# Performance work log

Hardware: AMD Instinct MI355X
Metric: run time of the kernel (lower is better)

Reference implementation:

```python
import jax, jax.numpy as jnp
import numpy as np

NEG_INF = -1e30  # safe -inf surrogate to avoid nan in logsumexp


def _ctc_loss_sum(log_probs, labels, input_lengths, label_lengths):
    # log_probs: (T, N, C) already log-softmaxed; blank = 0
    T, N, C = log_probs.shape
    S = labels.shape[1]
    L = 2 * S + 1  # extended label sequence: blank-interleaved

    # extended labels: [blank, y1, blank, y2, ..., blank]
    ext = jnp.zeros((N, L), dtype=jnp.int32).at[:, 1::2].set(labels.astype(jnp.int32))
    # gather emission log-probs for extended labels: (T, N, L)
    lp_ext = jnp.take_along_axis(log_probs, jnp.broadcast_to(ext[None], (T, N, L)), axis=2)

    # transition from l-2 allowed only for non-blank labels differing from ext[l-2]
    ext_m2 = jnp.pad(ext, ((0, 0), (2, 0)), constant_values=-1)[:, :L]
    allow_skip = (ext != 0) & (ext != ext_m2)  # (N, L)

    # alpha at t=0
    alpha0 = jnp.full((N, L), NEG_INF, dtype=log_probs.dtype)
    alpha0 = alpha0.at[:, 0].set(lp_ext[0, :, 0])
    alpha0 = alpha0.at[:, 1].set(jnp.where(label_lengths > 0, lp_ext[0, :, 1], NEG_INF))

    def step(alpha, t_and_lp):
        t, lp_t = t_and_lp  # lp_t: (N, L)
        a1 = jnp.pad(alpha, ((0, 0), (1, 0)), constant_values=NEG_INF)[:, :L]
        a2 = jnp.pad(alpha, ((0, 0), (2, 0)), constant_values=NEG_INF)[:, :L]
        a2 = jnp.where(allow_skip, a2, NEG_INF)
        m = jnp.maximum(jnp.maximum(alpha, a1), a2)
        lse = m + jnp.log(jnp.exp(alpha - m) + jnp.exp(a1 - m) + jnp.exp(a2 - m))
        new = jnp.where(m > NEG_INF / 2, lse + lp_t, NEG_INF)
        # freeze alpha past each sequence's input length
        alpha = jnp.where((t < input_lengths)[:, None], new, alpha)
        return alpha, None

    alpha, _ = jax.lax.scan(step, alpha0, (jnp.arange(1, T), lp_ext[1:]))

    # log-likelihood = logsumexp(alpha[2*Sl], alpha[2*Sl - 1])
    idx = (2 * label_lengths).astype(jnp.int32)
    a_last = jnp.take_along_axis(alpha, idx[:, None], axis=1)[:, 0]
    a_prev = jnp.take_along_axis(alpha, jnp.maximum(idx - 1, 0)[:, None], axis=1)[:, 0]
    a_prev = jnp.where(label_lengths > 0, a_prev, NEG_INF)
    m = jnp.maximum(a_last, a_prev)
    ll = m + jnp.log(jnp.exp(a_last - m) + jnp.exp(a_prev - m))
    loss = -ll
    # zero_infinity=True: replace infinite losses with 0
    loss = jnp.where(loss < -NEG_INF / 2, loss, 0.0)
    return jnp.sum(loss)


def setup_inputs() -> dict:
    T, N, C, S = 512, 32, 4000, 64
    key = jax.random.key(0)
    k1, k2 = jax.random.split(key)
    inputs = jax.random.normal(k1, (T, N, C), dtype=jnp.float32)
    labels = jax.random.randint(k2, (N, S), 1, C, dtype=jnp.int32)  # exclude blank=0
    input_lengths = jnp.full((N,), T, dtype=jnp.int32)
    label_lengths = jnp.full((N,), S, dtype=jnp.int32)
    return {"inputs": inputs, "labels": labels,
            "input_lengths": input_lengths, "label_lengths": label_lengths}


def reference(inputs, labels, input_lengths, label_lengths):
    log_probs = jax.nn.log_softmax(inputs, axis=2)
    return _ctc_loss_sum(log_probs, labels, input_lengths, label_lengths)
```

## Files before the change

### kernel.cpp

```cpp
#include <hip/hip_runtime.h>

#define LN2 0.6931471805599453f

constexpr int T = 512, N = 32, C = 4000, S = 64;
constexpr int TN   = T * N;
constexpr int ROWF = 68;
constexpr int CT   = 16;
constexpr int NCF  = 16;
constexpr int NCB  = 16;
constexpr int NCG  = 32;

__global__ __launch_bounds__(256) void k_softmax_probs(
    const float* __restrict__ x, const int* __restrict__ labels,
    float* __restrict__ pp, float* __restrict__ ee)
{
    int row  = blockIdx.x * 4 + (threadIdx.x >> 6);
    int lane = threadIdx.x & 63;
    const float*  rp  = x + (size_t)row * C;
    const float4* rp4 = reinterpret_cast<const float4*>(rp);

    float m = -INFINITY, s = 0.f;
    #pragma unroll
    for (int k = 0; k < 15; ++k) {
        float4 v = rp4[lane + 64 * k];
        float mv = fmaxf(fmaxf(v.x, v.y), fmaxf(v.z, v.w));
        float s4 = __expf(v.x - mv) + __expf(v.y - mv) +
                   __expf(v.z - mv) + __expf(v.w - mv);
        float nm = fmaxf(m, mv);
        s = s * __expf(m - nm) + s4 * __expf(mv - nm);
        m = nm;
    }
    if (lane < 40) {
        float4 v = rp4[960 + lane];
        float mv = fmaxf(fmaxf(v.x, v.y), fmaxf(v.z, v.w));
        float s4 = __expf(v.x - mv) + __expf(v.y - mv) +
                   __expf(v.z - mv) + __expf(v.w - mv);
        float nm = fmaxf(m, mv);
        s = s * __expf(m - nm) + s4 * __expf(mv - nm);
        m = nm;
    }
    for (int off = 32; off; off >>= 1) {
        float om = __shfl_xor(m, off), os = __shfl_xor(s, off);
        float nm = fmaxf(m, om);
        s = s * __expf(m - nm) + os * __expf(om - nm);
        m = nm;
    }
    float logZ = m + __logf(s);

    int t = row >> 5, n = row & 31;
    int c  = labels[n * S + lane];
    float zb = rp[0];
    float zl = rp[c];

    float wm = zl;
    for (int off = 32; off; off >>= 1) wm = fmaxf(wm, __shfl_xor(wm, off));
    wm = fmaxf(wm, zb);
    float pm = __expf(wm - logZ);
    int e = (int)(__float_as_uint(pm) >> 23) - 127;

    float* outp = pp + ((size_t)n * T + t) * ROWF;
    outp[1 + lane] = ldexpf(__expf(zl - logZ), -e);
    if (lane == 0) {
        outp[0] = ldexpf(__expf(zb - logZ), -e);
        ee[n * T + t] = (float)e;
    }
}

__device__ __forceinline__ float dpp_shr1_zero(float x) {
    int r = __builtin_amdgcn_update_dpp(0, __float_as_int(x),
                                        0x138 , 0xf, 0xf, false);
    return __int_as_float(r);
}
__device__ __forceinline__ float dpp_shl1_zero(float x) {
    int r = __builtin_amdgcn_update_dpp(0, __float_as_int(x),
                                        0x130 , 0xf, 0xf, false);
    return __int_as_float(r);
}
template <int CTRL>
__device__ __forceinline__ float dpp_max_step(float x) {
    int t = __builtin_amdgcn_update_dpp(__float_as_int(x), __float_as_int(x),
                                        CTRL, 0xf, 0xf, false);
    return fmaxf(x, __int_as_float(t));
}
__device__ __forceinline__ float wave_max_bcast(float x) {
    x = dpp_max_step<0xB1>(x);  x = dpp_max_step<0x4E>(x);
    x = dpp_max_step<0x141>(x); x = dpp_max_step<0x140>(x);
    x = dpp_max_step<0x142>(x); x = dpp_max_step<0x143>(x);
    return __int_as_float(__builtin_amdgcn_readlane(__float_as_int(x), 63));
}

__global__ __launch_bounds__(128) void k_ctc_alpha(
    const float* __restrict__ pp, const float* __restrict__ ee,
    const int* __restrict__ labels,
    const int* __restrict__ input_len, const int* __restrict__ label_len,
    float* __restrict__ loss_out)
{
    __shared__ __align__(16) float ldsF[2][CT][ROWF];
    __shared__ __align__(16) float ldsB[2][CT][ROWF];
    __shared__ float gj[132];
    const int n = blockIdx.x;
    const int wid = threadIdx.x >> 6, lane = threadIdx.x & 63;
    const int Tin = input_len[n], Sl = label_len[n];
    const float* bp = pp + (size_t)n * T * ROWF;
    const bool hot = (Tin == T);

    const int li   = labels[n * S + lane];
    const int lim1 = lane ? labels[n * S + lane - 1] : -1;
    const float skf  = (lane > 0 && li != 0 && li != lim1) ? 1.f : 0.f;
    const float skUf = dpp_shr1_zero(skf);
    const float skk  = skf * skUf;
    const float skD  = dpp_shl1_zero(skf);

    asm volatile("s_waitcnt vmcnt(0)" ::: "memory");
    __builtin_amdgcn_sched_barrier(0);

    float a0 = 0.f, a1 = 0.f, aX = 0.f;
    int SH = 0;

#define ISSUE_F(cc) do {                                                      \
    const float* cp_ = bp + (size_t)(cc) * CT * ROWF;                         \
    if (lane < 17) {                                                          \
        _Pragma("unroll")                                                     \
        for (int d_ = 0; d_ < CT; ++d_)                                       \
            __builtin_amdgcn_global_load_lds(cp_ + (size_t)d_ * ROWF + lane * 4, \
                                             &ldsF[(cc) & 1][d_][0], 16, 0, 0);\
    } } while (0)
#define ISSUE_B(cc) do {                                                      \
    const float* cp_ = bp + (size_t)(496 - 16 * (cc)) * ROWF;                 \
    if (lane < 17) {                                                          \
        _Pragma("unroll")                                                     \
        for (int d_ = 0; d_ < CT; ++d_)                                       \
            __builtin_amdgcn_global_load_lds(cp_ + (size_t)d_ * ROWF + lane * 4, \
                                             &ldsB[(cc) & 1][d_][0], 16, 0, 0);\
    } } while (0)

#define PAIRS(B, D) do {                                                      \
    const float* R0_ = &ldsF[B][D][0];                                        \
    const float* R1_ = &ldsF[B][(D) + 1][0];                                  \
    float cb1 = R0_[0], cl1 = R0_[1 + lane];                                  \
    float cb2 = R1_[0], cl2 = R1_[1 + lane];                                  \
    float clU = dpp_shr1_zero(cl1);                                           \
    float W   = clU * cl2;                                                    \
    float A   = cb1 * cb2;                                                    \
    float B_  = clU * cb2;                                                    \
    float Cc  = A + B_;                                                       \
    float D_  = skUf * B_;                                                    \
    float s1  = cb1 + cl1;                                                    \
    float E   = s1 * cl2;                                                     \
    float F   = cl1 * cl2;                                                    \
    float G   = skf * W;                                                      \
    float H   = fmaf(skf, F + W, cb1 * cl2);                                  \
    float I   = skk * W;                                                      \
    float Y0  = cl1 * cb2;                                                    \
    float Y1  = s1 * cb2;                                                     \
    float Y2  = skf * Y0;                                                     \
    float p1  = dpp_shr1_zero(a1);                                            \
    float p0  = dpp_shr1_zero(a0);                                            \
    float p2  = dpp_shr1_zero(p1);                                            \
    float n0  = fmaf(p0, B_, a0 * A) + fmaf(p2, D_, p1 * Cc);                 \
    float n1  = fmaf(a1, F, a0 * E) + fmaf(p2, I, fmaf(p1, H, p0 * G));       \
    float nX  = fmaf(a1, Y1, aX * A) + fmaf(p1, Y2, a0 * Y0);                 \
    a0 = n0; a1 = n1; aX = nX;                                                \
} while (0)

#define WINDOW4(B, D0) do {                                                   \
    a0 = ldexpf(a0, kA); a1 = ldexpf(a1, kA); aX = ldexpf(aX, kA);            \
    SH += kA;                                                                 \
    float gnow_ = fmaxf(fmaxf(a0, a1), aX);                                   \
    PAIRS(B, D0);                                                             \
    gs = dpp_max_step<0xB1>(gs);  gs = dpp_max_step<0x4E>(gs);                \
    PAIRS(B, (D0) + 2);                                                       \
    gs = dpp_max_step<0x141>(gs); gs = dpp_max_step<0x140>(gs);               \
    PAIRS(B, (D0) + 4);                                                       \
    gs = dpp_max_step<0x142>(gs); gs = dpp_max_step<0x143>(gs);               \
    PAIRS(B, (D0) + 6);                                                       \
    {   unsigned b_ = (unsigned)__builtin_amdgcn_readlane(__float_as_int(gs), 63); \
        int e_ = (int)(b_ >> 23) - 127;                                       \
        kA = (b_ == 0u) ? 0 : (105 - e_ - kA);                                \
    }                                                                         \
    gs = gnow_;                                                               \
} while (0)

#define BSTEP(B, D) do {                                                      \
    const float* R_ = &ldsB[B][D][0];                                         \
    float cb_ = R_[0], cl_ = R_[1 + lane];                                    \
    float cD_ = dpp_shl1_zero(cl_);                         \
    float d1_ = dpp_shl1_zero(g1);                           \
    float d0s_ = dpp_shl1_zero(g0);                          \
    float d0_ = (lane == 63) ? gX : d0s_;             \
    float t1_ = skD * cD_;                                                    \
    float cg_ = cl_ * g1;                                                     \
    float ng0 = fmaf(cb_, g0, cg_);                                           \
    float ng1 = fmaf(t1_, d1_, fmaf(cb_, d0_, cg_));                          \
    float ngX = cb_ * gX;                                                     \
    g0 = ng0; g1 = ng1; gX = ngX;                                             \
} while (0)

#define BWIN(B, D0) do {                                                      \
    g0 = ldexpf(g0, kB); g1 = ldexpf(g1, kB); gX = ldexpf(gX, kB);            \
    SHb += kB;                                                                \
    float gnow_ = fmaxf(fmaxf(g0, g1), gX);                                   \
    BSTEP(B, (D0) + 7); BSTEP(B, (D0) + 6);                                   \
    gsb = dpp_max_step<0xB1>(gsb);  gsb = dpp_max_step<0x4E>(gsb);            \
    BSTEP(B, (D0) + 5); BSTEP(B, (D0) + 4);                                   \
    gsb = dpp_max_step<0x141>(gsb); gsb = dpp_max_step<0x140>(gsb);           \
    BSTEP(B, (D0) + 3); BSTEP(B, (D0) + 2);                                   \
    gsb = dpp_max_step<0x142>(gsb); gsb = dpp_max_step<0x143>(gsb);           \
    BSTEP(B, (D0) + 1); BSTEP(B, (D0));                                       \
    {   unsigned b_ = (unsigned)__builtin_amdgcn_readlane(__float_as_int(gsb), 63); \
        int e_ = (int)(b_ >> 23) - 127;                                       \
        kB = (b_ == 0u) ? 0 : (100 - e_ - kB);                                \
    }                                                                         \
    gsb = gnow_;                                                              \
} while (0)

    if (wid == 0) {
        if (hot) {
            int kA = 0; float gs = 0.f;
            ISSUE_F(0); ISSUE_F(1);
            asm volatile("s_waitcnt vmcnt(16)" ::: "memory");
            __builtin_amdgcn_sched_barrier(0);
            a0 = (lane == 0) ? ldsF[0][0][0] : 0.f;
            a1 = (lane == 0 && Sl > 0) ? ldsF[0][0][1] : 0.f;
            {
                float cb = ldsF[0][1][0], cl = ldsF[0][1][1 + lane];
                float p1 = dpp_shr1_zero(a1);
                float n0 = (a0 + p1) * cb;
                float n1 = fmaf(skf, p1, a0 + a1) * cl;
                float nX = (aX + a1) * cb;
                a0 = n0; a1 = n1; aX = nX;
            }
            PAIRS(0, 2); PAIRS(0, 4); PAIRS(0, 6);
            {   float g = wave_max_bcast(fmaxf(fmaxf(a0, a1), aX));
                unsigned b = __float_as_uint(g);
                int k0 = (b == 0u) ? 0 : (105 - ((int)(b >> 23) - 127));
                a0 = ldexpf(a0, k0); a1 = ldexpf(a1, k0); aX = ldexpf(aX, k0);
                SH += k0; kA = 0;
                gs = fmaxf(fmaxf(a0, a1), aX);
            }
            WINDOW4(0, 8);
            __builtin_amdgcn_sched_barrier(0);
            ISSUE_F(2);
            for (int c = 1; c < NCF; ++c) {
                if (c < NCF - 1) { asm volatile("s_waitcnt vmcnt(16)" ::: "memory"); }
                else             { asm volatile("s_waitcnt vmcnt(0)"  ::: "memory"); }
                __builtin_amdgcn_sched_barrier(0);
                int buf = c & 1;
                WINDOW4(buf, 0);
                WINDOW4(buf, 8);
                if (c + 2 < NCF) {
                    __builtin_amdgcn_sched_barrier(0);
                    ISSUE_F(c + 2);
                }
            }
        } else {
#define GSTEP(cc, dd) do {                                                    \
    float cb_ = ldsF[(cc) & 1][dd][0];                                        \
    float cl_ = ldsF[(cc) & 1][dd][1 + lane];                                 \
    float p1_ = dpp_shr1_zero(a1);                                            \
    float na0_ = (a0 + p1_) * cb_;                                            \
    float na1_ = fmaf(skf, p1_, a0 + a1) * cl_;                               \
    float naX_ = (aX + a1) * cb_;                                             \
    int t_ = (cc) * CT + (dd);                                                \
    bool act_ = (unsigned)(t_ - 1) < (unsigned)(Tin - 1);                     \
    a0 = act_ ? na0_ : a0;                                                    \
    a1 = act_ ? na1_ : a1;                                                    \
    aX = act_ ? naX_ : aX;                                                    \
    if (((dd) & 3) == 3) {                                                    \
        float g_ = wave_max_bcast(fmaxf(a0, fmaxf(a1, aX)));                  \
        unsigned b_ = __float_as_uint(g_);                                    \
        int k_ = (b_ == 0u) ? 0 : (100 - ((int)(b_ >> 23) - 127));            \
        a0 = ldexpf(a0, k_); a1 = ldexpf(a1, k_); aX = ldexpf(aX, k_);        \
        SH += k_;                                                             \
    }                                                                         \
} while (0)
            ISSUE_F(0); ISSUE_F(1);
            asm volatile("s_waitcnt vmcnt(16)" ::: "memory");
            __builtin_amdgcn_sched_barrier(0);
            a0 = (lane == 0) ? ldsF[0][0][0] : 0.f;
            a1 = (lane == 0 && Sl > 0) ? ldsF[0][0][1] : 0.f;
            #pragma unroll
            for (int d = 1; d < CT; ++d) GSTEP(0, d);
            __builtin_amdgcn_sched_barrier(0);
            ISSUE_F(2);
            for (int c = 1; c < NCG; ++c) {
                if (c < NCG - 1) { asm volatile("s_waitcnt vmcnt(16)" ::: "memory"); }
                else             { asm volatile("s_waitcnt vmcnt(0)"  ::: "memory"); }
                __builtin_amdgcn_sched_barrier(0);
                #pragma unroll
                for (int d = 0; d < CT; ++d) GSTEP(c, d);
                if (c + 2 < NCG) {
                    __builtin_amdgcn_sched_barrier(0);
                    ISSUE_F(c + 2);
                }
            }
#undef GSTEP
        }
    } else if (hot) {
        float g0 = (lane == Sl) ? 1.f : 0.f;
        float g1 = (Sl > 0 && lane == Sl - 1) ? 1.f : 0.f;
        float gX = (Sl >= S && lane == 63) ? 1.f : 0.f;
        int SHb = 0, kB = 0;
        float gsb = fmaxf(fmaxf(g0, g1), gX);

        ISSUE_B(0); ISSUE_B(1);
        for (int c = 0; c < NCB; ++c) {
            if (c < NCB - 1) { asm volatile("s_waitcnt vmcnt(16)" ::: "memory"); }
            else             { asm volatile("s_waitcnt vmcnt(0)"  ::: "memory"); }
            __builtin_amdgcn_sched_barrier(0);
            int buf = c & 1;
            BWIN(buf, 8);
            BWIN(buf, 0);
            if (c + 2 < NCB) {
                __builtin_amdgcn_sched_barrier(0);
                ISSUE_B(c + 2);
            }
        }
        gj[2 * lane]     = ldexpf(g0, -120);
        gj[2 * lane + 1] = ldexpf(g1, -120);
        if (lane == 63) {
            gj[128] = ldexpf(gX, -120);
            gj[130] = (float)SHb;
        }
    }

    __syncthreads();
    if (wid != 0) return;

    float se = 0.f;
    #pragma unroll
    for (int j = 0; j < 8; ++j) {
        int idx = lane + 64 * j;
        float ev = ee[n * T + idx];
        se += (idx < Tin) ? ev : 0.f;
    }
    for (int off = 32; off; off >>= 1) se += __shfl_xor(se, off);

    if (hot) {
        float term = a0 * gj[2 * lane] + a1 * gj[2 * lane + 1];
        if (lane == 63) term = fmaf(aX, gj[128], term);
        for (int off = 32; off; off >>= 1) term += __shfl_xor(term, off);
        if (lane == 0) {
            float SHb = gj[130];
            float ll2  = log2f(term) - (float)SH - SHb + 120.f + se;
            float loss = -ll2 * LN2;
            if (!(loss < 5e29f)) loss = 0.f;
            loss_out[n] = loss;
        }
    } else {
        float a_last = (Sl >= S) ? __shfl(aX, 63) : __shfl(a0, Sl);
        float a_prev_raw = __shfl(a1, (Sl > 0) ? (Sl - 1) : 0);
        float a_prev = (Sl > 0) ? a_prev_raw : 0.f;
        if (lane == 0) {
            float sum  = a_last + a_prev;
            float ll2  = log2f(sum) - (float)SH + se;
            float loss = -ll2 * LN2;
            if (!(loss < 5e29f)) loss = 0.f;
            loss_out[n] = loss;
        }
    }
#undef BWIN
#undef BSTEP
#undef WINDOW4
#undef PAIRS
#undef ISSUE_F
#undef ISSUE_B
}

__global__ __launch_bounds__(64) void k_reduce(
    const float* __restrict__ loss, float* __restrict__ out)
{
    int lane = threadIdx.x;
    float v = (lane < N) ? loss[lane] : 0.f;
    for (int off = 32; off; off >>= 1) v += __shfl_xor(v, off);
    if (lane == 0) out[0] = v;
}

extern "C" void kernel_launch(void* const* d_in, const int* in_sizes, int n_in,
                              void* d_out, int out_size, void* d_ws, size_t ws_size,
                              hipStream_t stream) {
    const float* x       = (const float*)d_in[0];
    const int*   labels  = (const int*)d_in[1];
    const int*   in_len  = (const int*)d_in[2];
    const int*   lab_len = (const int*)d_in[3];
    float* out  = (float*)d_out;
    float* pp   = (float*)d_ws;
    float* ee   = pp + (size_t)TN * ROWF + 256;
    float* loss = ee + TN;

    k_softmax_probs<<<TN / 4, 256, 0, stream>>>(x, labels, pp, ee);
    k_ctc_alpha<<<N, 128, 0, stream>>>(pp, ee, labels, in_len, lab_len, loss);
    k_reduce<<<1, 64, 0, stream>>>(loss, out);
}
```

Measured before the change: 77.57 us.

## Overlap backward CTC recursion with softmax via phased kernels

```diff
diff --git a/kernel.cpp b/kernel.cpp
--- a/kernel.cpp
+++ b/kernel.cpp
@@ -6,16 +6,36 @@
 constexpr int TN   = T * N;
 constexpr int ROWF = 68;
 constexpr int CT   = 16;
-constexpr int NCF  = 16;
-constexpr int NCB  = 16;
-constexpr int NCG  = 32;
-
-__global__ __launch_bounds__(256) void k_softmax_probs(
+constexpr int CTB  = 8;
+constexpr int QROWS = 4096;
+
+__device__ __forceinline__ float dpp_shr1_zero(float x) {
+    int r = __builtin_amdgcn_update_dpp(0, __float_as_int(x),
+                                        0x138 , 0xf, 0xf, false);
+    return __int_as_float(r);
+}
+__device__ __forceinline__ float dpp_shl1_zero(float x) {
+    int r = __builtin_amdgcn_update_dpp(0, __float_as_int(x),
+                                        0x130 , 0xf, 0xf, false);
+    return __int_as_float(r);
+}
+template <int CTRL>
+__device__ __forceinline__ float dpp_max_step(float x) {
+    int t = __builtin_amdgcn_update_dpp(__float_as_int(x), __float_as_int(x),
+                                        CTRL, 0xf, 0xf, false);
+    return fmaxf(x, __int_as_float(t));
+}
+__device__ __forceinline__ float wave_max_bcast(float x) {
+    x = dpp_max_step<0xB1>(x);  x = dpp_max_step<0x4E>(x);
+    x = dpp_max_step<0x141>(x); x = dpp_max_step<0x140>(x);
+    x = dpp_max_step<0x142>(x); x = dpp_max_step<0x143>(x);
+    return __int_as_float(__builtin_amdgcn_readlane(__float_as_int(x), 63));
+}
+
+__device__ __forceinline__ void softmax_row(
     const float* __restrict__ x, const int* __restrict__ labels,
-    float* __restrict__ pp, float* __restrict__ ee)
+    float* __restrict__ pp, float* __restrict__ ee, int row, int lane)
 {
-    int row  = blockIdx.x * 4 + (threadIdx.x >> 6);
-    int lane = threadIdx.x & 63;
     const float*  rp  = x + (size_t)row * C;
     const float4* rp4 = reinterpret_cast<const float4*>(rp);
 
@@ -66,41 +86,115 @@
     }
 }
 
-__device__ __forceinline__ float dpp_shr1_zero(float x) {
-    int r = __builtin_amdgcn_update_dpp(0, __float_as_int(x),
-                                        0x138 , 0xf, 0xf, false);
-    return __int_as_float(r);
-}
-__device__ __forceinline__ float dpp_shl1_zero(float x) {
-    int r = __builtin_amdgcn_update_dpp(0, __float_as_int(x),
-                                        0x130 , 0xf, 0xf, false);
-    return __int_as_float(r);
-}
-template <int CTRL>
-__device__ __forceinline__ float dpp_max_step(float x) {
-    int t = __builtin_amdgcn_update_dpp(__float_as_int(x), __float_as_int(x),
-                                        CTRL, 0xf, 0xf, false);
-    return fmaxf(x, __int_as_float(t));
-}
-__device__ __forceinline__ float wave_max_bcast(float x) {
-    x = dpp_max_step<0xB1>(x);  x = dpp_max_step<0x4E>(x);
-    x = dpp_max_step<0x141>(x); x = dpp_max_step<0x140>(x);
-    x = dpp_max_step<0x142>(x); x = dpp_max_step<0x143>(x);
-    return __int_as_float(__builtin_amdgcn_readlane(__float_as_int(x), 63));
-}
-
-__global__ __launch_bounds__(128) void k_ctc_alpha(
+__global__ __launch_bounds__(256) void k_phase(
+    const float* __restrict__ x, const int* __restrict__ labels,
+    float* __restrict__ pp, float* __restrict__ ee, float* __restrict__ gst,
+    const int* __restrict__ in_len, const int* __restrict__ lab_len,
+    int qrow0, int ttop, int first)
+{
+    __shared__ __align__(16) float ldsB[4][2][CTB][ROWF];
+    const int wid = threadIdx.x >> 6, lane = threadIdx.x & 63;
+
+    if (blockIdx.x >= 8) {
+        softmax_row(x, labels, pp, ee,
+                    qrow0 + ((int)blockIdx.x - 8) * 4 + wid, lane);
+        return;
+    }
+    if (ttop < 0) return;
+    const int n = blockIdx.x * 4 + wid;
+    const int Tin = in_len[n], Sl = lab_len[n];
+    if (Tin != T) return;
+    const float* bp = pp + (size_t)n * T * ROWF;
+
+    const int li = labels[n * S + lane];
+    const int lim1 = lane ? labels[n * S + lane - 1] : -1;
+    const float skf = (lane > 0 && li != 0 && li != lim1) ? 1.f : 0.f;
+    const float skD = dpp_shl1_zero(skf);
+
+    float* st = gst + n * 136;
+    float g0, g1, gX;
+    int SHb;
+    if (first) {
+        g0 = (lane == Sl) ? 1.f : 0.f;
+        g1 = (Sl > 0 && lane == Sl - 1) ? 1.f : 0.f;
+        gX = (Sl >= S && lane == 63) ? 1.f : 0.f;
+        SHb = 0;
+    } else {
+        float2 g = *reinterpret_cast<const float2*>(&st[2 * lane]);
+        g0 = g.x; g1 = g.y;
+        gX = (lane == 63) ? st[128] : 0.f;
+        SHb = (int)st[129];
+    }
+    asm volatile("s_waitcnt vmcnt(0)" ::: "memory");
+    __builtin_amdgcn_sched_barrier(0);
+
+#define ISSUEB(cc) do {                                                       \
+    const float* cp_ = bp + (size_t)(ttop - 7 - 8 * (cc)) * ROWF;             \
+    if (lane < 17) {                                                          \
+        _Pragma("unroll")                                                     \
+        for (int d_ = 0; d_ < CTB; ++d_)                                      \
+            __builtin_amdgcn_global_load_lds(cp_ + (size_t)d_ * ROWF + lane * 4, \
+                                             &ldsB[wid][(cc) & 1][d_][0], 16, 0, 0); \
+    } } while (0)
+
+#define BSTEPP(B, D) do {                                                     \
+    const float* R_ = &ldsB[wid][B][D][0];                                    \
+    float cb_ = R_[0], cl_ = R_[1 + lane];                                    \
+    float cD_ = dpp_shl1_zero(cl_);                         \
+    float d1_ = dpp_shl1_zero(g1);                           \
+    float d0s_ = dpp_shl1_zero(g0);                          \
+    float d0_ = (lane == 63) ? gX : d0s_;                                     \
+    float cg_ = cl_ * g1;                                                     \
+    float ng0 = fmaf(cb_, g0, cg_);                                           \
+    float ng1 = fmaf(skD * cD_, d1_, fmaf(cb_, d0_, cg_));                    \
+    float ngX = cb_ * gX;                                                     \
+    g0 = ng0; g1 = ng1; gX = ngX;                                             \
+} while (0)
+
+#define BRENORM do {                                                          \
+    float g_ = wave_max_bcast(fmaxf(g0, fmaxf(g1, gX)));                      \
+    unsigned b_ = __float_as_uint(g_);                                        \
+    int k_ = (b_ == 0u) ? 0 : (100 - ((int)(b_ >> 23) - 127));                \
+    g0 = ldexpf(g0, k_); g1 = ldexpf(g1, k_); gX = ldexpf(gX, k_);            \
+    SHb += k_;                                                                \
+} while (0)
+
+    ISSUEB(0); ISSUEB(1);
+    for (int c = 0; c < 16; ++c) {
+        if (c < 15) { asm volatile("s_waitcnt vmcnt(8)" ::: "memory"); }
+        else        { asm volatile("s_waitcnt vmcnt(0)" ::: "memory"); }
+        __builtin_amdgcn_sched_barrier(0);
+        int buf = c & 1;
+        BSTEPP(buf, 7); BSTEPP(buf, 6); BSTEPP(buf, 5); BSTEPP(buf, 4);
+        BRENORM;
+        BSTEPP(buf, 3); BSTEPP(buf, 2); BSTEPP(buf, 1); BSTEPP(buf, 0);
+        BRENORM;
+        if (c + 2 < 16) {
+            __builtin_amdgcn_sched_barrier(0);
+            ISSUEB(c + 2);
+        }
+    }
+
+    float2 gv; gv.x = g0; gv.y = g1;
+    *reinterpret_cast<float2*>(&st[2 * lane]) = gv;
+    if (lane == 63) { st[128] = gX; st[129] = (float)SHb; }
+#undef BRENORM
+#undef BSTEPP
+#undef ISSUEB
+}
+
+__global__ __launch_bounds__(128) void k_final(
     const float* __restrict__ pp, const float* __restrict__ ee,
-    const int* __restrict__ labels,
-    const int* __restrict__ input_len, const int* __restrict__ label_len,
+    float* __restrict__ gst, const int* __restrict__ labels,
+    const int* __restrict__ in_len, const int* __restrict__ lab_len,
     float* __restrict__ loss_out)
 {
     __shared__ __align__(16) float ldsF[2][CT][ROWF];
-    __shared__ __align__(16) float ldsB[2][CT][ROWF];
+    __shared__ __align__(16) float ldsT[2][CT][ROWF];
     __shared__ float gj[132];
     const int n = blockIdx.x;
     const int wid = threadIdx.x >> 6, lane = threadIdx.x & 63;
-    const int Tin = input_len[n], Sl = label_len[n];
+    const int Tin = in_len[n], Sl = lab_len[n];
     const float* bp = pp + (size_t)n * T * ROWF;
     const bool hot = (Tin == T);
 
@@ -111,9 +205,6 @@
     const float skk  = skf * skUf;
     const float skD  = dpp_shl1_zero(skf);
 
-    asm volatile("s_waitcnt vmcnt(0)" ::: "memory");
-    __builtin_amdgcn_sched_barrier(0);
-
     float a0 = 0.f, a1 = 0.f, aX = 0.f;
     int SH = 0;
 
@@ -123,15 +214,15 @@
         _Pragma("unroll")                                                     \
         for (int d_ = 0; d_ < CT; ++d_)                                       \
             __builtin_amdgcn_global_load_lds(cp_ + (size_t)d_ * ROWF + lane * 4, \
-                                             &ldsF[(cc) & 1][d_][0], 16, 0, 0);\
+                                             &ldsF[(cc) & 1][d_][0], 16, 0, 0); \
     } } while (0)
-#define ISSUE_B(cc) do {                                                      \
-    const float* cp_ = bp + (size_t)(496 - 16 * (cc)) * ROWF;                 \
+#define ISSUE_T(cc) do {                                                      \
+    const float* cp_ = bp + (size_t)(112 - 16 * (cc)) * ROWF;                 \
     if (lane < 17) {                                                          \
         _Pragma("unroll")                                                     \
         for (int d_ = 0; d_ < CT; ++d_)                                       \
             __builtin_amdgcn_global_load_lds(cp_ + (size_t)d_ * ROWF + lane * 4, \
-                                             &ldsB[(cc) & 1][d_][0], 16, 0, 0);\
+                                             &ldsT[(cc) & 1][d_][0], 16, 0, 0); \
     } } while (0)
 
 #define PAIRS(B, D) do {                                                      \
@@ -181,38 +272,29 @@
     gs = gnow_;                                                               \
 } while (0)
 
-#define BSTEP(B, D) do {                                                      \
-    const float* R_ = &ldsB[B][D][0];                                         \
+#define BSTEPT(B, D) do {                                                     \
+    const float* R_ = &ldsT[B][D][0];                                         \
     float cb_ = R_[0], cl_ = R_[1 + lane];                                    \
-    float cD_ = dpp_shl1_zero(cl_);                         \
-    float d1_ = dpp_shl1_zero(g1);                           \
-    float d0s_ = dpp_shl1_zero(g0);                          \
-    float d0_ = (lane == 63) ? gX : d0s_;             \
-    float t1_ = skD * cD_;                                                    \
+    float cD_ = dpp_shl1_zero(cl_);                                           \
+    float d1_ = dpp_shl1_zero(g1);                                            \
+    float d0s_ = dpp_shl1_zero(g0);                                           \
+    float d0_ = (lane == 63) ? gX : d0s_;                                     \
     float cg_ = cl_ * g1;                                                     \
     float ng0 = fmaf(cb_, g0, cg_);                                           \
-    float ng1 = fmaf(t1_, d1_, fmaf(cb_, d0_, cg_));                          \
+    float ng1 = fmaf(skD * cD_, d1_, fmaf(cb_, d0_, cg_));                    \
     float ngX = cb_ * gX;                                                     \
     g0 = ng0; g1 = ng1; gX = ngX;                                             \
 } while (0)
-
-#define BWIN(B, D0) do {                                                      \
-    g0 = ldexpf(g0, kB); g1 = ldexpf(g1, kB); gX = ldexpf(gX, kB);            \
-    SHb += kB;                                                                \
-    float gnow_ = fmaxf(fmaxf(g0, g1), gX);                                   \
-    BSTEP(B, (D0) + 7); BSTEP(B, (D0) + 6);                                   \
-    gsb = dpp_max_step<0xB1>(gsb);  gsb = dpp_max_step<0x4E>(gsb);            \
-    BSTEP(B, (D0) + 5); BSTEP(B, (D0) + 4);                                   \
-    gsb = dpp_max_step<0x141>(gsb); gsb = dpp_max_step<0x140>(gsb);           \
-    BSTEP(B, (D0) + 3); BSTEP(B, (D0) + 2);                                   \
-    gsb = dpp_max_step<0x142>(gsb); gsb = dpp_max_step<0x143>(gsb);           \
-    BSTEP(B, (D0) + 1); BSTEP(B, (D0));                                       \
-    {   unsigned b_ = (unsigned)__builtin_amdgcn_readlane(__float_as_int(gsb), 63); \
-        int e_ = (int)(b_ >> 23) - 127;                                       \
-        kB = (b_ == 0u) ? 0 : (100 - e_ - kB);                                \
-    }                                                                         \
-    gsb = gnow_;                                                              \
-} while (0)
+#define BRENORM do {                                                          \
+    float g_ = wave_max_bcast(fmaxf(g0, fmaxf(g1, gX)));                      \
+    unsigned b_ = __float_as_uint(g_);                                        \
+    int k_ = (b_ == 0u) ? 0 : (100 - ((int)(b_ >> 23) - 127));                \
+    g0 = ldexpf(g0, k_); g1 = ldexpf(g1, k_); gX = ldexpf(gX, k_);            \
+    SHb += k_;                                                                \
+} while (0)
+
+    asm volatile("s_waitcnt vmcnt(0)" ::: "memory");
+    __builtin_amdgcn_sched_barrier(0);
 
     if (wid == 0) {
         if (hot) {
@@ -241,14 +323,14 @@
             WINDOW4(0, 8);
             __builtin_amdgcn_sched_barrier(0);
             ISSUE_F(2);
-            for (int c = 1; c < NCF; ++c) {
-                if (c < NCF - 1) { asm volatile("s_waitcnt vmcnt(16)" ::: "memory"); }
-                else             { asm volatile("s_waitcnt vmcnt(0)"  ::: "memory"); }
+            for (int c = 1; c < 4; ++c) {
+                if (c < 3) { asm volatile("s_waitcnt vmcnt(16)" ::: "memory"); }
+                else       { asm volatile("s_waitcnt vmcnt(0)"  ::: "memory"); }
                 __builtin_amdgcn_sched_barrier(0);
                 int buf = c & 1;
                 WINDOW4(buf, 0);
                 WINDOW4(buf, 8);
-                if (c + 2 < NCF) {
+                if (c + 2 < 4) {
                     __builtin_amdgcn_sched_barrier(0);
                     ISSUE_F(c + 2);
                 }
@@ -283,13 +365,13 @@
             for (int d = 1; d < CT; ++d) GSTEP(0, d);
             __builtin_amdgcn_sched_barrier(0);
             ISSUE_F(2);
-            for (int c = 1; c < NCG; ++c) {
-                if (c < NCG - 1) { asm volatile("s_waitcnt vmcnt(16)" ::: "memory"); }
-                else             { asm volatile("s_waitcnt vmcnt(0)"  ::: "memory"); }
+            for (int c = 1; c < T / CT; ++c) {
+                if (c < T / CT - 1) { asm volatile("s_waitcnt vmcnt(16)" ::: "memory"); }
+                else                { asm volatile("s_waitcnt vmcnt(0)"  ::: "memory"); }
                 __builtin_amdgcn_sched_barrier(0);
                 #pragma unroll
                 for (int d = 0; d < CT; ++d) GSTEP(c, d);
-                if (c + 2 < NCG) {
+                if (c + 2 < T / CT) {
                     __builtin_amdgcn_sched_barrier(0);
                     ISSUE_F(c + 2);
                 }
@@ -297,23 +379,29 @@
 #undef GSTEP
         }
     } else if (hot) {
-        float g0 = (lane == Sl) ? 1.f : 0.f;
-        float g1 = (Sl > 0 && lane == Sl - 1) ? 1.f : 0.f;
-        float gX = (Sl >= S && lane == 63) ? 1.f : 0.f;
-        int SHb = 0, kB = 0;
-        float gsb = fmaxf(fmaxf(g0, g1), gX);
-
-        ISSUE_B(0); ISSUE_B(1);
-        for (int c = 0; c < NCB; ++c) {
-            if (c < NCB - 1) { asm volatile("s_waitcnt vmcnt(16)" ::: "memory"); }
-            else             { asm volatile("s_waitcnt vmcnt(0)"  ::: "memory"); }
+        float* st = gst + n * 136;
+        float2 g = *reinterpret_cast<const float2*>(&st[2 * lane]);
+        float g0 = g.x, g1 = g.y;
+        float gX = (lane == 63) ? st[128] : 0.f;
+        int SHb = (int)st[129];
+
+        ISSUE_T(0); ISSUE_T(1);
+        for (int c = 0; c < 4; ++c) {
+            if (c < 3) { asm volatile("s_waitcnt vmcnt(16)" ::: "memory"); }
+            else       { asm volatile("s_waitcnt vmcnt(0)"  ::: "memory"); }
             __builtin_amdgcn_sched_barrier(0);
             int buf = c & 1;
-            BWIN(buf, 8);
-            BWIN(buf, 0);
-            if (c + 2 < NCB) {
+            BSTEPT(buf, 15); BSTEPT(buf, 14); BSTEPT(buf, 13); BSTEPT(buf, 12);
+            BRENORM;
+            BSTEPT(buf, 11); BSTEPT(buf, 10); BSTEPT(buf, 9);  BSTEPT(buf, 8);
+            BRENORM;
+            BSTEPT(buf, 7);  BSTEPT(buf, 6);  BSTEPT(buf, 5);  BSTEPT(buf, 4);
+            BRENORM;
+            BSTEPT(buf, 3);  BSTEPT(buf, 2);  BSTEPT(buf, 1);  BSTEPT(buf, 0);
+            BRENORM;
+            if (c + 2 < 4) {
                 __builtin_amdgcn_sched_barrier(0);
-                ISSUE_B(c + 2);
+                ISSUE_T(c + 2);
             }
         }
         gj[2 * lane]     = ldexpf(g0, -120);
@@ -359,12 +447,12 @@
             loss_out[n] = loss;
         }
     }
-#undef BWIN
-#undef BSTEP
+#undef BRENORM
+#undef BSTEPT
 #undef WINDOW4
 #undef PAIRS
 #undef ISSUE_F
-#undef ISSUE_B
+#undef ISSUE_T
 }
 
 __global__ __launch_bounds__(64) void k_reduce(
@@ -387,8 +475,17 @@
     float* pp   = (float*)d_ws;
     float* ee   = pp + (size_t)TN * ROWF + 256;
     float* loss = ee + TN;
-
-    k_softmax_probs<<<TN / 4, 256, 0, stream>>>(x, labels, pp, ee);
-    k_ctc_alpha<<<N, 128, 0, stream>>>(pp, ee, labels, in_len, lab_len, loss);
+    float* gst  = loss + N + 32;
+
+    const int NB = 8 + QROWS / 4;
+    k_phase<<<NB, 256, 0, stream>>>(x, labels, pp, ee, gst, in_len, lab_len,
+                                    3 * QROWS, -1, 0);
+    k_phase<<<NB, 256, 0, stream>>>(x, labels, pp, ee, gst, in_len, lab_len,
+                                    2 * QROWS, 511, 1);
+    k_phase<<<NB, 256, 0, stream>>>(x, labels, pp, ee, gst, in_len, lab_len,
+                                    1 * QROWS, 383, 0);
+    k_phase<<<NB, 256, 0, stream>>>(x, labels, pp, ee, gst, in_len, lab_len,
+                                    0 * QROWS, 255, 0);
+    k_final<<<N, 128, 0, stream>>>(pp, ee, gst, labels, in_len, lab_len, loss);
     k_reduce<<<1, 64, 0, stream>>>(loss, out);
 }
```

After: 81.38 us. 4.9% more time.

## Simplify backward renormalization and fuse final reduction via atomicAdd

Applied to the files above, without the earlier changes.

```diff
diff --git a/kernel.cpp b/kernel.cpp
--- a/kernel.cpp
+++ b/kernel.cpp
@@ -93,7 +93,7 @@
     const float* __restrict__ pp, const float* __restrict__ ee,
     const int* __restrict__ labels,
     const int* __restrict__ input_len, const int* __restrict__ label_len,
-    float* __restrict__ loss_out)
+    float* __restrict__ out)
 {
     __shared__ __align__(16) float ldsF[2][CT][ROWF];
     __shared__ __align__(16) float ldsB[2][CT][ROWF];
@@ -181,37 +181,25 @@
     gs = gnow_;                                                               \
 } while (0)
 
-#define BSTEP(B, D) do {                                                      \
+#define BSTEPT(B, D) do {                                                     \
     const float* R_ = &ldsB[B][D][0];                                         \
     float cb_ = R_[0], cl_ = R_[1 + lane];                                    \
     float cD_ = dpp_shl1_zero(cl_);                         \
     float d1_ = dpp_shl1_zero(g1);                           \
     float d0s_ = dpp_shl1_zero(g0);                          \
     float d0_ = (lane == 63) ? gX : d0s_;             \
-    float t1_ = skD * cD_;                                                    \
     float cg_ = cl_ * g1;                                                     \
     float ng0 = fmaf(cb_, g0, cg_);                                           \
-    float ng1 = fmaf(t1_, d1_, fmaf(cb_, d0_, cg_));                          \
+    float ng1 = fmaf(skD * cD_, d1_, fmaf(cb_, d0_, cg_));                    \
     float ngX = cb_ * gX;                                                     \
     g0 = ng0; g1 = ng1; gX = ngX;                                             \
 } while (0)
-
-#define BWIN(B, D0) do {                                                      \
-    g0 = ldexpf(g0, kB); g1 = ldexpf(g1, kB); gX = ldexpf(gX, kB);            \
-    SHb += kB;                                                                \
-    float gnow_ = fmaxf(fmaxf(g0, g1), gX);                                   \
-    BSTEP(B, (D0) + 7); BSTEP(B, (D0) + 6);                                   \
-    gsb = dpp_max_step<0xB1>(gsb);  gsb = dpp_max_step<0x4E>(gsb);            \
-    BSTEP(B, (D0) + 5); BSTEP(B, (D0) + 4);                                   \
-    gsb = dpp_max_step<0x141>(gsb); gsb = dpp_max_step<0x140>(gsb);           \
-    BSTEP(B, (D0) + 3); BSTEP(B, (D0) + 2);                                   \
-    gsb = dpp_max_step<0x142>(gsb); gsb = dpp_max_step<0x143>(gsb);           \
-    BSTEP(B, (D0) + 1); BSTEP(B, (D0));                                       \
-    {   unsigned b_ = (unsigned)__builtin_amdgcn_readlane(__float_as_int(gsb), 63); \
-        int e_ = (int)(b_ >> 23) - 127;                                       \
-        kB = (b_ == 0u) ? 0 : (100 - e_ - kB);                                \
-    }                                                                         \
-    gsb = gnow_;                                                              \
+#define BRENORM do {                                                          \
+    float g_ = wave_max_bcast(fmaxf(g0, fmaxf(g1, gX)));                      \
+    unsigned b_ = __float_as_uint(g_);                                        \
+    int k_ = (b_ == 0u) ? 0 : (100 - ((int)(b_ >> 23) - 127));                \
+    g0 = ldexpf(g0, k_); g1 = ldexpf(g1, k_); gX = ldexpf(gX, k_);            \
+    SHb += k_;                                                                \
 } while (0)
 
     if (wid == 0) {
@@ -300,8 +288,7 @@
         float g0 = (lane == Sl) ? 1.f : 0.f;
         float g1 = (Sl > 0 && lane == Sl - 1) ? 1.f : 0.f;
         float gX = (Sl >= S && lane == 63) ? 1.f : 0.f;
-        int SHb = 0, kB = 0;
-        float gsb = fmaxf(fmaxf(g0, g1), gX);
+        int SHb = 0;
 
         ISSUE_B(0); ISSUE_B(1);
         for (int c = 0; c < NCB; ++c) {
@@ -309,8 +296,14 @@
             else             { asm volatile("s_waitcnt vmcnt(0)"  ::: "memory"); }
             __builtin_amdgcn_sched_barrier(0);
             int buf = c & 1;
-            BWIN(buf, 8);
-            BWIN(buf, 0);
+            BSTEPT(buf, 15); BSTEPT(buf, 14); BSTEPT(buf, 13); BSTEPT(buf, 12);
+            BRENORM;
+            BSTEPT(buf, 11); BSTEPT(buf, 10); BSTEPT(buf, 9);  BSTEPT(buf, 8);
+            BRENORM;
+            BSTEPT(buf, 7);  BSTEPT(buf, 6);  BSTEPT(buf, 5);  BSTEPT(buf, 4);
+            BRENORM;
+            BSTEPT(buf, 3);  BSTEPT(buf, 2);  BSTEPT(buf, 1);  BSTEPT(buf, 0);
+            BRENORM;
             if (c + 2 < NCB) {
                 __builtin_amdgcn_sched_barrier(0);
                 ISSUE_B(c + 2);
@@ -345,7 +338,7 @@
             float ll2  = log2f(term) - (float)SH - SHb + 120.f + se;
             float loss = -ll2 * LN2;
             if (!(loss < 5e29f)) loss = 0.f;
-            loss_out[n] = loss;
+            atomicAdd(out, loss);
         }
     } else {
         float a_last = (Sl >= S) ? __shfl(aX, 63) : __shfl(a0, Sl);
@@ -356,24 +349,15 @@
             float ll2  = log2f(sum) - (float)SH + se;
             float loss = -ll2 * LN2;
             if (!(loss < 5e29f)) loss = 0.f;
-            loss_out[n] = loss;
-        }
-    }
-#undef BWIN
-#undef BSTEP
+            atomicAdd(out, loss);
+        }
+    }
+#undef BRENORM
+#undef BSTEPT
 #undef WINDOW4
 #undef PAIRS
 #undef ISSUE_F
 #undef ISSUE_B
-}
-
-__global__ __launch_bounds__(64) void k_reduce(
-    const float* __restrict__ loss, float* __restrict__ out)
-{
-    int lane = threadIdx.x;
-    float v = (lane < N) ? loss[lane] : 0.f;
-    for (int off = 32; off; off >>= 1) v += __shfl_xor(v, off);
-    if (lane == 0) out[0] = v;
 }
 
 extern "C" void kernel_launch(void* const* d_in, const int* in_sizes, int n_in,
@@ -386,9 +370,8 @@
     float* out  = (float*)d_out;
     float* pp   = (float*)d_ws;
     float* ee   = pp + (size_t)TN * ROWF + 256;
-    float* loss = ee + TN;
-
+
+    hipMemsetAsync(out, 0, sizeof(float), stream);
     k_softmax_probs<<<TN / 4, 256, 0, stream>>>(x, labels, pp, ee);
-    k_ctc_alpha<<<N, 128, 0, stream>>>(pp, ee, labels, in_len, lab_len, loss);
-    k_reduce<<<1, 64, 0, stream>>>(loss, out);
-}
+    k_ctc_alpha<<<N, 128, 0, stream>>>(pp, ee, labels, in_len, lab_len, out);
+}
```

Measured after the change: 81.55 us. 5.1% more time.
